# Kernel optimization log

Measured on AMD Instinct MI355X. Metric: run time of the kernel, lower is better.

## Reference

```python
import jax, jax.numpy as jnp
import numpy as np

NEG_INF = jnp.float32(-1e30)


def setup_inputs() -> dict:
    key = jax.random.key(0)
    ks = jax.random.split(key, 7)
    B, Lx, Lm, d = 4, 256, 256, 256
    return {
        "x": jax.random.normal(ks[0], (B, Lx, d), dtype=jnp.float32),
        "memory": jax.random.normal(ks[1], (B, Lm, d), dtype=jnp.float32),
        "memory_mask": jax.random.randint(ks[2], (B, Lm), 0, 2, dtype=jnp.int32),
        "ws1_w": jax.random.normal(ks[3], (d, d), dtype=jnp.float32) * 0.05,
        "ws1_b": jax.random.normal(ks[4], (d,), dtype=jnp.float32) * 0.05,
        "ws2_w": jax.random.normal(ks[5], (d, d), dtype=jnp.float32) * 0.05,
        "wst_w": jax.random.normal(ks[6], (1, d), dtype=jnp.float32) * 0.05,
    }


def reference(x, memory, memory_mask, ws1_w, ws1_b, ws2_w, wst_w):
    # x: [B, Lx, d], memory: [B, Lm, d]; torch Linear: y = x @ W.T + b
    item1 = jnp.einsum('bxd,ed->bxe', x, ws1_w) + ws1_b          # [B, Lx, d]
    item2 = jnp.einsum('bmd,ed->bme', memory, ws2_w)             # [B, Lm, d]
    item = jnp.tanh(item1[:, :, None, :] + item2[:, None, :, :])  # [B, Lx, Lm, d]
    S = jnp.einsum('bxmd,d->bxm', item, wst_w[0])                # [B, Lx, Lm]
    # agg_2_h uses the UNMASKED scores, softmax over Lx after transpose
    agg_2_h = jnp.einsum('bmx,bxd->bmd', jax.nn.softmax(S.transpose(0, 2, 1), axis=-1), x)
    # mask applied to S before the main attention readout
    S = jnp.where(memory_mask[:, None, :] == 0, NEG_INF, S)      # [B, Lx, Lm]
    out = jnp.einsum('bxm,bmd->bxd', jax.nn.softmax(S, axis=-1), memory)
    return (out, S, agg_2_h)
```

## Files before the change

### kernel.cpp

```cpp
#include <hip/hip_runtime.h>

static constexpr int NB = 4;
static constexpr int L  = 256;
static constexpr int D  = 256;

__device__ __forceinline__ float fast_rcp(float x) {
#if __has_builtin(__builtin_amdgcn_rcpf)
    return __builtin_amdgcn_rcpf(x);
#else
    return 1.0f / x;
#endif
}

__device__ __forceinline__ float fast_exp(float x) {
#if __has_builtin(__builtin_amdgcn_exp2f)
    return __builtin_amdgcn_exp2f(x * 1.4426950408889634f);
#else
    return __expf(x);
#endif
}

__device__ __forceinline__ float tanh_fast(float y) {
#if __has_builtin(__builtin_amdgcn_exp2f)
    float e = __builtin_amdgcn_exp2f(y * 2.8853900817779268f);
#else
    float e = __expf(2.0f * y);
#endif
    return fmaf(-2.0f, fast_rcp(e + 1.0f), 1.0f);
}

__global__ __launch_bounds__(256) void linear_kernel(
    const float* __restrict__ x, const float* __restrict__ mem,
    const float* __restrict__ w1, const float* __restrict__ b1,
    const float* __restrict__ w2,
    float* __restrict__ i1, float* __restrict__ i2)
{
    const int bid = blockIdx.x;
    const int rb  = (bid >> 3) * 32;
    const int cb  = (bid & 7) * 32;
    const int which = rb >= 1024;
    const int rloc  = which ? rb - 1024 : rb;
    const float* src = which ? mem : x;
    const float* W   = which ? w2  : w1;
    float*       dst = which ? i2  : i1;

    constexpr int P4 = 65;
    __shared__ __align__(16) float4 xs4[32 * P4];
    __shared__ __align__(16) float4 ws4[32 * P4];

    const int t = threadIdx.x;
    const float4* src4 = reinterpret_cast<const float4*>(src) + rloc * 64;
    const float4* Wg4  = reinterpret_cast<const float4*>(W)   + cb   * 64;
#pragma unroll
    for (int k = 0; k < 8; ++k) {
        int idx = k * 256 + t;
        int r = idx >> 6, c = idx & 63;
        xs4[r * P4 + c] = src4[r * 64 + c];
        ws4[r * P4 + c] = Wg4[r * 64 + c];
    }
    __syncthreads();

    const int rr = t >> 4, cc = t & 15;
    const float4* a0p = xs4 + rr * P4;
    const float4* a1p = xs4 + (rr + 16) * P4;
    const float4* w0p = ws4 + cc * P4;
    const float4* w1p = ws4 + (cc + 16) * P4;
    float acc00 = 0.f, acc01 = 0.f, acc10 = 0.f, acc11 = 0.f;
#pragma unroll 4
    for (int d4 = 0; d4 < 64; ++d4) {
        float4 a0 = a0p[d4], a1 = a1p[d4];
        float4 w0 = w0p[d4], w1 = w1p[d4];
        acc00 = fmaf(a0.x, w0.x, acc00); acc00 = fmaf(a0.y, w0.y, acc00);
        acc00 = fmaf(a0.z, w0.z, acc00); acc00 = fmaf(a0.w, w0.w, acc00);
        acc01 = fmaf(a0.x, w1.x, acc01); acc01 = fmaf(a0.y, w1.y, acc01);
        acc01 = fmaf(a0.z, w1.z, acc01); acc01 = fmaf(a0.w, w1.w, acc01);
        acc10 = fmaf(a1.x, w0.x, acc10); acc10 = fmaf(a1.y, w0.y, acc10);
        acc10 = fmaf(a1.z, w0.z, acc10); acc10 = fmaf(a1.w, w0.w, acc10);
        acc11 = fmaf(a1.x, w1.x, acc11); acc11 = fmaf(a1.y, w1.y, acc11);
        acc11 = fmaf(a1.z, w1.z, acc11); acc11 = fmaf(a1.w, w1.w, acc11);
    }
    const float bias0 = which ? 0.f : b1[cb + cc];
    const float bias1 = which ? 0.f : b1[cb + cc + 16];
    dst[(rloc + rr)      * D + cb + cc]      = acc00 + bias0;
    dst[(rloc + rr)      * D + cb + cc + 16] = acc01 + bias1;
    dst[(rloc + rr + 16) * D + cb + cc]      = acc10 + bias0;
    dst[(rloc + rr + 16) * D + cb + cc + 16] = acc11 + bias1;
}

__global__ __launch_bounds__(256) void score_kernel(
    const float* __restrict__ i1, const float* __restrict__ i2,
    const float* __restrict__ wst, const int* __restrict__ mask,
    float* __restrict__ outS, float* __restrict__ ST)
{
    const int bid = blockIdx.x;
    const int b   = bid >> 8;
    const int xt  = ((bid >> 4) & 15) * 16;
    const int mt  = (bid & 15) * 16;
    const int t   = threadIdx.x;

    constexpr int PAD = 260;
    __shared__ __align__(16) float s1[16 * PAD];
    __shared__ __align__(16) float s2[16 * PAD];
    __shared__ float stile[16 * 17];

    const float4* i14 = reinterpret_cast<const float4*>(i1) + (b * L + xt) * (D / 4);
    const float4* i24 = reinterpret_cast<const float4*>(i2) + (b * L + mt) * (D / 4);
    float4* s14 = reinterpret_cast<float4*>(s1);
    float4* s24 = reinterpret_cast<float4*>(s2);
#pragma unroll
    for (int k = 0; k < 4; ++k) {
        int idx = k * 256 + t;
        int r = idx >> 6, c = idx & 63;
        s14[r * (PAD / 4) + c] = i14[r * (D / 4) + c];
        s24[r * (PAD / 4) + c] = i24[r * (D / 4) + c];
    }
    __syncthreads();

    const int xl = t >> 4, ml = t & 15;
    const float4* a4 = s14 + xl * (PAD / 4);
    const float4* b4 = s24 + ml * (PAD / 4);
    const float4* w4 = reinterpret_cast<const float4*>(wst);
    float acc = 0.0f;
#pragma unroll 4
    for (int d4 = 0; d4 < D / 4; ++d4) {
        float4 a  = a4[d4];
        float4 bb = b4[d4];
        float4 w  = w4[d4];
        acc = fmaf(tanh_fast(a.x + bb.x), w.x, acc);
        acc = fmaf(tanh_fast(a.y + bb.y), w.y, acc);
        acc = fmaf(tanh_fast(a.z + bb.z), w.z, acc);
        acc = fmaf(tanh_fast(a.w + bb.w), w.w, acc);
    }
    const int xi = xt + xl, mi = mt + ml;
    outS[((b * L + xi) << 8) + mi] = (mask[b * L + mi] == 0) ? -1e30f : acc;

    stile[ml * 17 + xl] = acc;
    __syncthreads();
    const int m2 = t >> 4, x2 = t & 15;
    ST[((b * L + mt + m2) << 8) + xt + x2] = stile[m2 * 17 + x2];
}

__global__ __launch_bounds__(256) void attn_kernel(
    const float* __restrict__ S1, const float* __restrict__ V1, float* __restrict__ out1,
    const float* __restrict__ S2, const float* __restrict__ V2, float* __restrict__ out2)
{
    int bid = blockIdx.x;
    const float* S; const float* V; float* out;
    if (bid < NB * L / 4) { S = S1; V = V1; out = out1; }
    else                  { S = S2; V = V2; out = out2; bid -= NB * L / 4; }

    const int row0 = bid * 4;
    const int b    = row0 >> 8;
    const int t    = threadIdx.x;
    const int w    = t >> 6, l = t & 63;

    __shared__ __align__(16) float p[4][L];
    __shared__ __align__(16) float4 part[4][4][64];

    {
        float4 sv = reinterpret_cast<const float4*>(S)[((row0 + w) << 6) + l];
        float m = fmaxf(fmaxf(sv.x, sv.y), fmaxf(sv.z, sv.w));
#pragma unroll
        for (int o = 32; o; o >>= 1) m = fmaxf(m, __shfl_xor(m, o));
        float e0 = fast_exp(sv.x - m), e1 = fast_exp(sv.y - m);
        float e2 = fast_exp(sv.z - m), e3 = fast_exp(sv.w - m);
        float s = (e0 + e1) + (e2 + e3);
#pragma unroll
        for (int o = 32; o; o >>= 1) s += __shfl_xor(s, o);
        float rs = fast_rcp(s);
        reinterpret_cast<float4*>(p[w])[l] = make_float4(e0 * rs, e1 * rs, e2 * rs, e3 * rs);
    }
    __syncthreads();

    const float4* V4 = reinterpret_cast<const float4*>(V) + (b * L) * (D / 4);
    float4 acc[4];
#pragma unroll
    for (int r = 0; r < 4; ++r) acc[r] = make_float4(0.f, 0.f, 0.f, 0.f);

#pragma unroll 4
    for (int k = 0; k < 64; ++k) {
        int mm = w * 64 + k;
        float4 v = V4[mm * (D / 4) + l];
#pragma unroll
        for (int r = 0; r < 4; ++r) {
            float pm = p[r][mm];
            acc[r].x = fmaf(pm, v.x, acc[r].x);
            acc[r].y = fmaf(pm, v.y, acc[r].y);
            acc[r].z = fmaf(pm, v.z, acc[r].z);
            acc[r].w = fmaf(pm, v.w, acc[r].w);
        }
    }
#pragma unroll
    for (int r = 0; r < 4; ++r) part[r][w][l] = acc[r];
    __syncthreads();

    {
        float4 r0 = part[w][0][l], r1 = part[w][1][l];
        float4 r2 = part[w][2][l], r3 = part[w][3][l];
        float4 o;
        o.x = (r0.x + r1.x) + (r2.x + r3.x);
        o.y = (r0.y + r1.y) + (r2.y + r3.y);
        o.z = (r0.z + r1.z) + (r2.z + r3.z);
        o.w = (r0.w + r1.w) + (r2.w + r3.w);
        reinterpret_cast<float4*>(out)[((row0 + w) << 6) + l] = o;
    }
}

extern "C" void kernel_launch(void* const* d_in, const int* in_sizes, int n_in,
                              void* d_out, int out_size, void* d_ws, size_t ws_size,
                              hipStream_t stream)
{
    const float* x    = (const float*)d_in[0];
    const float* mem  = (const float*)d_in[1];
    const int*   mask = (const int*)  d_in[2];
    const float* w1   = (const float*)d_in[3];
    const float* b1   = (const float*)d_in[4];
    const float* w2   = (const float*)d_in[5];
    const float* wst  = (const float*)d_in[6];

    float* out   = (float*)d_out;
    float* Smask = out + NB * L * L;
    float* agg   = Smask + NB * L * L;

    float* i1 = (float*)d_ws;
    float* i2 = i1 + NB * L * D;
    float* ST = i2 + NB * L * D;

    linear_kernel<<<512, 256, 0, stream>>>(x, mem, w1, b1, w2, i1, i2);
    score_kernel<<<NB * (L / 16) * (L / 16), 256, 0, stream>>>(i1, i2, wst, mask, Smask, ST);
    attn_kernel<<<2 * (NB * L / 4), 256, 0, stream>>>(Smask, mem, out, ST, x, agg);
}
```

Measured before the change: 39.88 us.

## Fuse score and attention kernels, precompute exp factors in interleaved layout

The linear kernel now stores exp(2*item) in a d-plane-interleaved layout, so tanh(a+b) becomes a multiply of two stored exponentials plus a reciprocal, which removes one exp per element. The score and softmax/readout kernels are merged into one kernel: each block computes four full score rows (or columns for the transposed path), masks them, applies softmax in shared memory and multiplies by V. This drops the ST intermediate and one launch. The cost is that the score work is done twice (once per direction), the ex*ey product can overflow for large inputs, and fewer, heavier blocks run.

Result: slower. 42.82 us (+7.4%).

```diff
diff --git a/kernel.cpp b/kernel.cpp
--- a/kernel.cpp
+++ b/kernel.cpp
@@ -20,12 +20,15 @@
 #endif
 }
 
-__device__ __forceinline__ float tanh_fast(float y) {
+__device__ __forceinline__ float exp_2x(float x) {
 #if __has_builtin(__builtin_amdgcn_exp2f)
-    float e = __builtin_amdgcn_exp2f(y * 2.8853900817779268f);
+    return __builtin_amdgcn_exp2f(x * 2.8853900817779268f);
 #else
-    float e = __expf(2.0f * y);
+    return __expf(2.0f * x);
 #endif
+}
+
+__device__ __forceinline__ float tanh_from_e(float e) {
     return fmaf(-2.0f, fast_rcp(e + 1.0f), 1.0f);
 }
 
@@ -33,7 +36,7 @@
     const float* __restrict__ x, const float* __restrict__ mem,
     const float* __restrict__ w1, const float* __restrict__ b1,
     const float* __restrict__ w2,
-    float* __restrict__ i1, float* __restrict__ i2)
+    float* __restrict__ E1X, float* __restrict__ E2X)
 {
     const int bid = blockIdx.x;
     const int rb  = (bid >> 3) * 32;
@@ -42,7 +45,7 @@
     const int rloc  = which ? rb - 1024 : rb;
     const float* src = which ? mem : x;
     const float* W   = which ? w2  : w1;
-    float*       dst = which ? i2  : i1;
+    float*       dstX = which ? E2X : E1X;
 
     constexpr int P4 = 65;
     __shared__ __align__(16) float4 xs4[32 * P4];
@@ -81,84 +84,86 @@
     }
     const float bias0 = which ? 0.f : b1[cb + cc];
     const float bias1 = which ? 0.f : b1[cb + cc + 16];
-    dst[(rloc + rr)      * D + cb + cc]      = acc00 + bias0;
-    dst[(rloc + rr)      * D + cb + cc + 16] = acc01 + bias1;
-    dst[(rloc + rr + 16) * D + cb + cc]      = acc10 + bias0;
-    dst[(rloc + rr + 16) * D + cb + cc + 16] = acc11 + bias1;
-}
-
-__global__ __launch_bounds__(256) void score_kernel(
-    const float* __restrict__ i1, const float* __restrict__ i2,
-    const float* __restrict__ wst, const int* __restrict__ mask,
-    float* __restrict__ outS, float* __restrict__ ST)
-{
-    const int bid = blockIdx.x;
-    const int b   = bid >> 8;
-    const int xt  = ((bid >> 4) & 15) * 16;
-    const int mt  = (bid & 15) * 16;
-    const int t   = threadIdx.x;
-
-    constexpr int PAD = 260;
-    __shared__ __align__(16) float s1[16 * PAD];
-    __shared__ __align__(16) float s2[16 * PAD];
-    __shared__ float stile[16 * 17];
-
-    const float4* i14 = reinterpret_cast<const float4*>(i1) + (b * L + xt) * (D / 4);
-    const float4* i24 = reinterpret_cast<const float4*>(i2) + (b * L + mt) * (D / 4);
-    float4* s14 = reinterpret_cast<float4*>(s1);
-    float4* s24 = reinterpret_cast<float4*>(s2);
-#pragma unroll
-    for (int k = 0; k < 4; ++k) {
-        int idx = k * 256 + t;
-        int r = idx >> 6, c = idx & 63;
-        s14[r * (PAD / 4) + c] = i14[r * (D / 4) + c];
-        s24[r * (PAD / 4) + c] = i24[r * (D / 4) + c];
-    }
-    __syncthreads();
-
-    const int xl = t >> 4, ml = t & 15;
-    const float4* a4 = s14 + xl * (PAD / 4);
-    const float4* b4 = s24 + ml * (PAD / 4);
-    const float4* w4 = reinterpret_cast<const float4*>(wst);
-    float acc = 0.0f;
-#pragma unroll 4
-    for (int d4 = 0; d4 < D / 4; ++d4) {
-        float4 a  = a4[d4];
-        float4 bb = b4[d4];
-        float4 w  = w4[d4];
-        acc = fmaf(tanh_fast(a.x + bb.x), w.x, acc);
-        acc = fmaf(tanh_fast(a.y + bb.y), w.y, acc);
-        acc = fmaf(tanh_fast(a.z + bb.z), w.z, acc);
-        acc = fmaf(tanh_fast(a.w + bb.w), w.w, acc);
-    }
-    const int xi = xt + xl, mi = mt + ml;
-    outS[((b * L + xi) << 8) + mi] = (mask[b * L + mi] == 0) ? -1e30f : acc;
-
-    stile[ml * 17 + xl] = acc;
-    __syncthreads();
-    const int m2 = t >> 4, x2 = t & 15;
-    ST[((b * L + mt + m2) << 8) + xt + x2] = stile[m2 * 17 + x2];
-}
-
-__global__ __launch_bounds__(256) void attn_kernel(
-    const float* __restrict__ S1, const float* __restrict__ V1, float* __restrict__ out1,
-    const float* __restrict__ S2, const float* __restrict__ V2, float* __restrict__ out2)
+    const float e00 = exp_2x(acc00 + bias0);
+    const float e01 = exp_2x(acc01 + bias1);
+    const float e10 = exp_2x(acc10 + bias0);
+    const float e11 = exp_2x(acc11 + bias1);
+    const int c0 = cb + cc, c1 = cb + cc + 16;
+    const int rA = rloc + rr, rB = rloc + rr + 16;
+    dstX[((c0 >> 2) * 1024 + rA) * 4 + (c0 & 3)] = e00;
+    dstX[((c1 >> 2) * 1024 + rA) * 4 + (c1 & 3)] = e01;
+    dstX[((c0 >> 2) * 1024 + rB) * 4 + (c0 & 3)] = e10;
+    dstX[((c1 >> 2) * 1024 + rB) * 4 + (c1 & 3)] = e11;
+}
+
+__global__ __launch_bounds__(256) void fused2_kernel(
+    const float* __restrict__ x, const float* __restrict__ mem,
+    const int* __restrict__ mask, const float* __restrict__ wst,
+    const float* __restrict__ E1X, const float* __restrict__ E2X,
+    float* __restrict__ out, float* __restrict__ Smask, float* __restrict__ agg)
 {
     int bid = blockIdx.x;
-    const float* S; const float* V; float* out;
-    if (bid < NB * L / 4) { S = S1; V = V1; out = out1; }
-    else                  { S = S2; V = V2; out = out2; bid -= NB * L / 4; }
-
-    const int row0 = bid * 4;
-    const int b    = row0 >> 8;
+    const bool isRow = bid < 256;
+    if (!isRow) bid -= 256;
+    const int b    = bid >> 6;
+    const int r0   = (bid & 63) * 4;
+    const int base = b * L;
     const int t    = threadIdx.x;
-    const int w    = t >> 6, l = t & 63;
-
-    __shared__ __align__(16) float p[4][L];
+
+    const float4* laneE  = reinterpret_cast<const float4*>(isRow ? E2X : E1X);
+    const float4* stripE = reinterpret_cast<const float4*>(isRow ? E1X : E2X);
+    const float4* w4     = reinterpret_cast<const float4*>(wst);
+
+    float acc0 = 0.f, acc1 = 0.f, acc2 = 0.f, acc3 = 0.f;
+#pragma unroll 4
+    for (int d4 = 0; d4 < 64; ++d4) {
+        const int plane = d4 * 1024 + base;
+        float4 ev = laneE[plane + t];
+        float4 s0 = stripE[plane + r0];
+        float4 s1 = stripE[plane + r0 + 1];
+        float4 s2 = stripE[plane + r0 + 2];
+        float4 s3 = stripE[plane + r0 + 3];
+        float4 w  = w4[d4];
+        acc0 = fmaf(tanh_from_e(ev.x * s0.x), w.x, acc0);
+        acc0 = fmaf(tanh_from_e(ev.y * s0.y), w.y, acc0);
+        acc0 = fmaf(tanh_from_e(ev.z * s0.z), w.z, acc0);
+        acc0 = fmaf(tanh_from_e(ev.w * s0.w), w.w, acc0);
+        acc1 = fmaf(tanh_from_e(ev.x * s1.x), w.x, acc1);
+        acc1 = fmaf(tanh_from_e(ev.y * s1.y), w.y, acc1);
+        acc1 = fmaf(tanh_from_e(ev.z * s1.z), w.z, acc1);
+        acc1 = fmaf(tanh_from_e(ev.w * s1.w), w.w, acc1);
+        acc2 = fmaf(tanh_from_e(ev.x * s2.x), w.x, acc2);
+        acc2 = fmaf(tanh_from_e(ev.y * s2.y), w.y, acc2);
+        acc2 = fmaf(tanh_from_e(ev.z * s2.z), w.z, acc2);
+        acc2 = fmaf(tanh_from_e(ev.w * s2.w), w.w, acc2);
+        acc3 = fmaf(tanh_from_e(ev.x * s3.x), w.x, acc3);
+        acc3 = fmaf(tanh_from_e(ev.y * s3.y), w.y, acc3);
+        acc3 = fmaf(tanh_from_e(ev.z * s3.z), w.z, acc3);
+        acc3 = fmaf(tanh_from_e(ev.w * s3.w), w.w, acc3);
+    }
+
+    __shared__ __align__(16) float sS[4][L];
     __shared__ __align__(16) float4 part[4][4][64];
 
+    if (isRow) {
+        const bool dead = (mask[base + t] == 0);
+        const float v0 = dead ? -1e30f : acc0;
+        const float v1 = dead ? -1e30f : acc1;
+        const float v2 = dead ? -1e30f : acc2;
+        const float v3 = dead ? -1e30f : acc3;
+        Smask[((base + r0 + 0) << 8) + t] = v0;
+        Smask[((base + r0 + 1) << 8) + t] = v1;
+        Smask[((base + r0 + 2) << 8) + t] = v2;
+        Smask[((base + r0 + 3) << 8) + t] = v3;
+        sS[0][t] = v0; sS[1][t] = v1; sS[2][t] = v2; sS[3][t] = v3;
+    } else {
+        sS[0][t] = acc0; sS[1][t] = acc1; sS[2][t] = acc2; sS[3][t] = acc3;
+    }
+    __syncthreads();
+
+    const int w = t >> 6, l = t & 63;
     {
-        float4 sv = reinterpret_cast<const float4*>(S)[((row0 + w) << 6) + l];
+        float4 sv = reinterpret_cast<const float4*>(sS[w])[l];
         float m = fmaxf(fmaxf(sv.x, sv.y), fmaxf(sv.z, sv.w));
 #pragma unroll
         for (int o = 32; o; o >>= 1) m = fmaxf(m, __shfl_xor(m, o));
@@ -168,26 +173,34 @@
 #pragma unroll
         for (int o = 32; o; o >>= 1) s += __shfl_xor(s, o);
         float rs = fast_rcp(s);
-        reinterpret_cast<float4*>(p[w])[l] = make_float4(e0 * rs, e1 * rs, e2 * rs, e3 * rs);
-    }
-    __syncthreads();
-
-    const float4* V4 = reinterpret_cast<const float4*>(V) + (b * L) * (D / 4);
+        reinterpret_cast<float4*>(sS[w])[l] =
+            make_float4(e0 * rs, e1 * rs, e2 * rs, e3 * rs);
+    }
+    __syncthreads();
+
+    const float4* V4 = reinterpret_cast<const float4*>(isRow ? mem : x) + base * 64;
     float4 acc[4];
 #pragma unroll
     for (int r = 0; r < 4; ++r) acc[r] = make_float4(0.f, 0.f, 0.f, 0.f);
 
-#pragma unroll 4
-    for (int k = 0; k < 64; ++k) {
-        int mm = w * 64 + k;
-        float4 v = V4[mm * (D / 4) + l];
+#pragma unroll 2
+    for (int k4 = 0; k4 < 16; ++k4) {
+        const int m0 = w * 64 + k4 * 4;
+        float4 v0 = V4[(m0 + 0) * 64 + l];
+        float4 v1 = V4[(m0 + 1) * 64 + l];
+        float4 v2 = V4[(m0 + 2) * 64 + l];
+        float4 v3 = V4[(m0 + 3) * 64 + l];
 #pragma unroll
         for (int r = 0; r < 4; ++r) {
-            float pm = p[r][mm];
-            acc[r].x = fmaf(pm, v.x, acc[r].x);
-            acc[r].y = fmaf(pm, v.y, acc[r].y);
-            acc[r].z = fmaf(pm, v.z, acc[r].z);
-            acc[r].w = fmaf(pm, v.w, acc[r].w);
+            float4 pr = *reinterpret_cast<const float4*>(&sS[r][m0]);
+            acc[r].x = fmaf(pr.x, v0.x, acc[r].x); acc[r].y = fmaf(pr.x, v0.y, acc[r].y);
+            acc[r].z = fmaf(pr.x, v0.z, acc[r].z); acc[r].w = fmaf(pr.x, v0.w, acc[r].w);
+            acc[r].x = fmaf(pr.y, v1.x, acc[r].x); acc[r].y = fmaf(pr.y, v1.y, acc[r].y);
+            acc[r].z = fmaf(pr.y, v1.z, acc[r].z); acc[r].w = fmaf(pr.y, v1.w, acc[r].w);
+            acc[r].x = fmaf(pr.z, v2.x, acc[r].x); acc[r].y = fmaf(pr.z, v2.y, acc[r].y);
+            acc[r].z = fmaf(pr.z, v2.z, acc[r].z); acc[r].w = fmaf(pr.z, v2.w, acc[r].w);
+            acc[r].x = fmaf(pr.w, v3.x, acc[r].x); acc[r].y = fmaf(pr.w, v3.y, acc[r].y);
+            acc[r].z = fmaf(pr.w, v3.z, acc[r].z); acc[r].w = fmaf(pr.w, v3.w, acc[r].w);
         }
     }
 #pragma unroll
@@ -195,14 +208,15 @@
     __syncthreads();
 
     {
-        float4 r0 = part[w][0][l], r1 = part[w][1][l];
-        float4 r2 = part[w][2][l], r3 = part[w][3][l];
-        float4 o;
-        o.x = (r0.x + r1.x) + (r2.x + r3.x);
-        o.y = (r0.y + r1.y) + (r2.y + r3.y);
-        o.z = (r0.z + r1.z) + (r2.z + r3.z);
-        o.w = (r0.w + r1.w) + (r2.w + r3.w);
-        reinterpret_cast<float4*>(out)[((row0 + w) << 6) + l] = o;
+        float4 q0 = part[w][0][l], q1 = part[w][1][l];
+        float4 q2 = part[w][2][l], q3 = part[w][3][l];
+        float4 ov;
+        ov.x = (q0.x + q1.x) + (q2.x + q3.x);
+        ov.y = (q0.y + q1.y) + (q2.y + q3.y);
+        ov.z = (q0.z + q1.z) + (q2.z + q3.z);
+        ov.w = (q0.w + q1.w) + (q2.w + q3.w);
+        float* o = isRow ? out : agg;
+        reinterpret_cast<float4*>(o)[((base + r0 + w) << 6) + l] = ov;
     }
 }
 
@@ -222,11 +236,10 @@
     float* Smask = out + NB * L * L;
     float* agg   = Smask + NB * L * L;
 
-    float* i1 = (float*)d_ws;
-    float* i2 = i1 + NB * L * D;
-    float* ST = i2 + NB * L * D;
-
-    linear_kernel<<<512, 256, 0, stream>>>(x, mem, w1, b1, w2, i1, i2);
-    score_kernel<<<NB * (L / 16) * (L / 16), 256, 0, stream>>>(i1, i2, wst, mask, Smask, ST);
-    attn_kernel<<<2 * (NB * L / 4), 256, 0, stream>>>(Smask, mem, out, ST, x, agg);
-}
+    float* E1X = (float*)d_ws;
+    float* E2X = E1X + NB * L * D;
+
+    linear_kernel<<<512, 256, 0, stream>>>(x, mem, w1, b1, w2, E1X, E2X);
+    fused2_kernel<<<512, 256, 0, stream>>>(x, mem, mask, wst, E1X, E2X,
+                                           out, Smask, agg);
+}
```
